# Performance work log

Measured on AMD Instinct MI355X. Metric: run time of the kernel, lower is better.

Reference implementation:

```python
import jax, jax.numpy as jnp
import numpy as np

TOP_K = 2
CAPACITY_FACTOR = 1.25
LOAD_BALANCE_WEIGHT = 0.01
ROUTER_Z_WEIGHT = 0.001


def setup_inputs() -> dict:
    key = jax.random.key(0)
    k1, k2, k3, k4, k5 = jax.random.split(key, 5)
    B, S, D, F, E = 4, 2048, 1024, 4096, 8
    x = jax.random.normal(k1, (B, S, D), dtype=jnp.float32)
    gate_w = jax.random.normal(k2, (E, D), dtype=jnp.float32) * 0.02
    wi_gate = jax.random.normal(k3, (E, F, D), dtype=jnp.float32) * 0.02
    wi_up = jax.random.normal(k4, (E, F, D), dtype=jnp.float32) * 0.02
    wo = jax.random.normal(k5, (E, D, F), dtype=jnp.float32) * 0.02
    return {"x": x, "gate_w": gate_w, "wi_gate": wi_gate, "wi_up": wi_up, "wo": wo}


def _dispatch_combine_one_k(x_flat, eids, ew, wi_gate, wi_up, wo, capacity):
    """Capacity-limited dispatch (first-come positions), GeGLU expert, combine."""
    N, D = x_flat.shape
    E = wi_gate.shape[0]
    # position of each token within its expert's queue (count of earlier tokens
    # assigned to the same expert) -- matches the atomic counter semantics in order.
    oh = jax.nn.one_hot(eids, E, dtype=jnp.int32)            # [N, E]
    pos = jnp.cumsum(oh, axis=0) - oh                        # counts strictly before
    pos = jnp.take_along_axis(pos, eids[:, None], axis=1)[:, 0]  # [N]
    valid = pos < capacity
    pos_safe = jnp.where(valid, pos, capacity)               # overflow bucket
    # dispatched_x[e, c, :] = x of the token at slot (e, c); zeros where empty
    disp = jnp.zeros((E, capacity + 1, D), x_flat.dtype).at[eids, pos_safe].set(x_flat)
    disp = disp[:, :capacity]                                # drop overflow bucket
    # grouped GeGLU expert: batched GEMMs over experts
    gate_h = jax.nn.silu(jnp.einsum('ecd,efd->ecf', disp, wi_gate))
    up_h = jnp.einsum('ecd,efd->ecf', disp, wi_up)
    eout = jnp.einsum('ecf,edf->ecd', gate_h * up_h, wo)     # [E, cap, D]
    # combine: gather each token's expert output, weight, zero dropped tokens
    y = eout[eids, jnp.minimum(pos, capacity - 1)]           # [N, D]
    return y * (ew * valid.astype(x_flat.dtype))[:, None]


def reference(x, gate_w, wi_gate, wi_up, wo):
    B, S, D = x.shape
    E = gate_w.shape[0]
    N = B * S
    capacity = max(int(N / E * CAPACITY_FACTOR), 1)
    x_flat = x.reshape(N, D)
    router_logits = x_flat @ gate_w.T                        # [N, E]
    router_probs = jax.nn.softmax(router_logits, axis=-1)
    topk_probs, topk_idx = jax.lax.top_k(router_probs, TOP_K)
    topk_probs = topk_probs / jnp.sum(topk_probs, axis=-1, keepdims=True)
    out = jnp.zeros_like(x_flat)
    for k in range(TOP_K):
        out = out + _dispatch_combine_one_k(
            x_flat, topk_idx[:, k], topk_probs[:, k], wi_gate, wi_up, wo, capacity)
    # aux losses: Switch-style load balance + router z-loss
    density = jnp.mean(jax.nn.one_hot(topk_idx, E, dtype=x.dtype).sum(axis=1), axis=0) / TOP_K
    mean_probs = jnp.mean(router_probs, axis=0)
    lb_loss = LOAD_BALANCE_WEIGHT * E * jnp.sum(density * mean_probs)
    z_loss = ROUTER_Z_WEIGHT * jnp.mean(jax.scipy.special.logsumexp(router_logits, axis=-1) ** 2)
    aux_loss = lb_loss + z_loss
    return out.reshape(B, S, D), aux_loss
```

## Files before the change

kernel.cpp:

```cpp
#include <hip/hip_runtime.h>
#include <cstdint>
#include <cstddef>

#define N_TOK 8192
#define DDIM  1024
#define FDIM  4096
#define NEXP  8
#define CAP   1280
#define MPE   2560
#define NSLOT (NEXP * MPE)

typedef __attribute__((ext_vector_type(8))) __bf16 bf16x8;
typedef __attribute__((ext_vector_type(4))) float  f32x4;

__device__ __forceinline__ unsigned short f2bf(float f) {
    unsigned int u = __float_as_uint(f);
    u += 0x7fffu + ((u >> 16) & 1u);
    return (unsigned short)(u >> 16);
}
__device__ __forceinline__ float bf2f(unsigned short s) {
    unsigned int u = ((unsigned int)s) << 16;
    return __uint_as_float(u);
}

__device__ __forceinline__ void async_cp16(const void* g, void* l) {
    __builtin_amdgcn_global_load_lds(
        (const __attribute__((address_space(1))) unsigned int*)g,
        (__attribute__((address_space(3))) unsigned int*)l, 16, 0, 0);
}

__global__ __launch_bounds__(256) void convert_wi_kernel(
    const float* __restrict__ wi_gate, const float* __restrict__ wi_up,
    unsigned short* __restrict__ wcomb)
{
    const int idx = blockIdx.x * 256 + threadIdx.x;
    const int d8 = idx & 127;
    const int r  = (idx >> 7) & 8191;
    const int e  = idx >> 20;
    const int f  = (r >> 7) * 64 + (r & 63);
    const float* src = (((r >> 6) & 1) ? wi_up : wi_gate)
                       + ((size_t)(e * FDIM + f) * DDIM + d8 * 8);
    const float4 a = ((const float4*)src)[0];
    const float4 b = ((const float4*)src)[1];
    uint4 o;
    o.x = (unsigned)f2bf(a.x) | ((unsigned)f2bf(a.y) << 16);
    o.y = (unsigned)f2bf(a.z) | ((unsigned)f2bf(a.w) << 16);
    o.z = (unsigned)f2bf(b.x) | ((unsigned)f2bf(b.y) << 16);
    o.w = (unsigned)f2bf(b.z) | ((unsigned)f2bf(b.w) << 16);
    *(uint4*)(wcomb + (size_t)idx * 8) = o;
}

__global__ __launch_bounds__(256) void convert_wo_kernel(
    const float* __restrict__ wo, unsigned short* __restrict__ wo_bf)
{
    const int idx = blockIdx.x * 256 + threadIdx.x;
    const float4 a = ((const float4*)(wo + (size_t)idx * 8))[0];
    const float4 b = ((const float4*)(wo + (size_t)idx * 8))[1];
    uint4 o;
    o.x = (unsigned)f2bf(a.x) | ((unsigned)f2bf(a.y) << 16);
    o.y = (unsigned)f2bf(a.z) | ((unsigned)f2bf(a.w) << 16);
    o.z = (unsigned)f2bf(b.x) | ((unsigned)f2bf(b.y) << 16);
    o.w = (unsigned)f2bf(b.z) | ((unsigned)f2bf(b.w) << 16);
    *(uint4*)(wo_bf + (size_t)idx * 8) = o;
}

__global__ __launch_bounds__(256) void router_kernel(
    const float* __restrict__ x, const float* __restrict__ gate_w,
    int* __restrict__ topk_idx, float* __restrict__ topk_w,
    float* __restrict__ stats)
{
    __shared__ float red[256][9];
    const int n = blockIdx.x;
    const int t = threadIdx.x;
    const float4 xv = *(const float4*)(x + (size_t)n * DDIM + t * 4);
#pragma unroll
    for (int e = 0; e < NEXP; e++) {
        const float4 gv = *(const float4*)(gate_w + (size_t)e * DDIM + t * 4);
        red[t][e] = xv.x * gv.x + xv.y * gv.y + xv.z * gv.z + xv.w * gv.w;
    }
    __syncthreads();
    for (int s = 128; s > 0; s >>= 1) {
        if (t < s) {
#pragma unroll
            for (int e = 0; e < NEXP; e++) red[t][e] += red[t + s][e];
        }
        __syncthreads();
    }
    if (t == 0) {
        float l[NEXP], p[NEXP];
        float m = -1e30f;
#pragma unroll
        for (int e = 0; e < NEXP; e++) { l[e] = red[0][e]; m = fmaxf(m, l[e]); }
        float sum = 0.f;
#pragma unroll
        for (int e = 0; e < NEXP; e++) { p[e] = expf(l[e] - m); sum += p[e]; }
        const float inv = 1.f / sum;
#pragma unroll
        for (int e = 0; e < NEXP; e++) p[e] *= inv;
        const float lse = m + logf(sum);
        int e1 = 0; float p1 = p[0];
#pragma unroll
        for (int e = 1; e < NEXP; e++) if (p[e] > p1) { p1 = p[e]; e1 = e; }
        int e2 = -1; float p2 = -1.f;
#pragma unroll
        for (int e = 0; e < NEXP; e++) if (e != e1 && p[e] > p2) { p2 = p[e]; e2 = e; }
        const float wsum = p1 + p2;
        topk_idx[n * 2 + 0] = e1; topk_idx[n * 2 + 1] = e2;
        topk_w[n * 2 + 0] = p1 / wsum; topk_w[n * 2 + 1] = p2 / wsum;
        float* sp = stats + (n & 63) * 17;
#pragma unroll
        for (int e = 0; e < NEXP; e++) atomicAdd(sp + e, p[e]);
        atomicAdd(sp + 8 + e1, 1.f);
        atomicAdd(sp + 8 + e2, 1.f);
        atomicAdd(sp + 16, lse * lse);
    }
}

__global__ __launch_bounds__(512) void pos_kernel(
    const int* __restrict__ topk_idx, const float* __restrict__ topk_w,
    int* __restrict__ slot_tok, float* __restrict__ w_slot, int* __restrict__ gcnt)
{
    __shared__ int cnt[2][NEXP][256];
    const int t = threadIdx.x;
    for (int i = t; i < NSLOT; i += 512) { slot_tok[i] = -1; w_slot[i] = 0.f; }
    const int kk = t >> 8;
    const int c  = t & 255;
    int lc[NEXP];
#pragma unroll
    for (int e = 0; e < NEXP; e++) lc[e] = 0;
    const int base_n = c * 32;
    for (int i = 0; i < 32; i++) lc[topk_idx[(base_n + i) * 2 + kk]]++;
#pragma unroll
    for (int e = 0; e < NEXP; e++) cnt[kk][e][c] = lc[e];
    __syncthreads();
    if (t < 16) {
        const int k2 = t >> 3, e = t & 7;
        int run = 0;
        for (int c2 = 0; c2 < 256; c2++) { int v = cnt[k2][e][c2]; cnt[k2][e][c2] = run; run += v; }
        gcnt[e * 2 + k2] = run < CAP ? run : CAP;
    }
    __syncthreads();
    int run[NEXP];
#pragma unroll
    for (int e = 0; e < NEXP; e++) run[e] = cnt[kk][e][c];
    for (int i = 0; i < 32; i++) {
        const int n = base_n + i;
        const int e = topk_idx[n * 2 + kk];
        const int p = run[e]++;
        if (p < CAP) {
            const int slot = (e * 2 + kk) * CAP + p;
            slot_tok[slot] = n;
            w_slot[slot] = topk_w[n * 2 + kk];
        }
    }
}

__global__ __launch_bounds__(128) void dispatch_kernel(
    const float* __restrict__ x, const int* __restrict__ slot_tok,
    unsigned short* __restrict__ disp)
{
    const int slot = blockIdx.x;
    const int t = threadIdx.x;
    const int token = slot_tok[slot];
    uint4 o = make_uint4(0u, 0u, 0u, 0u);
    if (token >= 0) {
        const float4* src = (const float4*)(x + (size_t)token * DDIM + t * 8);
        const float4 a = src[0];
        const float4 b = src[1];
        o.x = (unsigned)f2bf(a.x) | ((unsigned)f2bf(a.y) << 16);
        o.y = (unsigned)f2bf(a.z) | ((unsigned)f2bf(a.w) << 16);
        o.z = (unsigned)f2bf(b.x) | ((unsigned)f2bf(b.y) << 16);
        o.w = (unsigned)f2bf(b.z) | ((unsigned)f2bf(b.w) << 16);
    }
    *(uint4*)(disp + (size_t)slot * DDIM + t * 8) = o;
}

__global__ __launch_bounds__(256, 3) void gemm1_kernel(
    const unsigned short* __restrict__ disp,
    const unsigned short* __restrict__ wcomb,
    const int* __restrict__ gcnt,
    unsigned short* __restrict__ act)
{
    __shared__ __align__(16) unsigned short smem[8192];
    const int b = blockIdx.x;
    const int e   = b / 1280;
    const int rem = b % 1280;
    const int mb = rem / 64, nb = rem % 64;
    const int kk = mb / 10;
    if ((mb % 10) * 128 >= gcnt[e * 2 + kk]) return;

    const int t = threadIdx.x;
    const int wave = t >> 6, lane = t & 63;
    const unsigned short* Asrc = disp  + (size_t)(e * MPE + mb * 128) * DDIM;
    const unsigned short* Bsrc = wcomb + (size_t)e * 8192 * DDIM + (size_t)(nb * 128) * DDIM;

    const int arow = t >> 2;
    const int acol = (t & 3) * 8;

    const f32x4 fzero = {0.f, 0.f, 0.f, 0.f};
    f32x4 acc[4][4];
#pragma unroll
    for (int i = 0; i < 4; i++)
#pragma unroll
        for (int j = 0; j < 4; j++) acc[i][j] = fzero;

    const int wm = wave >> 1, wn = wave & 1;
    const int lrow = lane & 15, lk = lane >> 4;

    for (int k0 = 0; k0 < DDIM; k0 += 32) {
        __syncthreads();
        async_cp16(Asrc + (size_t)arow * DDIM + k0 + acol,        &smem[wave * 512]);
        async_cp16(Asrc + (size_t)(arow + 64) * DDIM + k0 + acol, &smem[2048 + wave * 512]);
        async_cp16(Bsrc + (size_t)arow * DDIM + k0 + acol,        &smem[4096 + wave * 512]);
        async_cp16(Bsrc + (size_t)(arow + 64) * DDIM + k0 + acol, &smem[6144 + wave * 512]);
        __syncthreads();
        bf16x8 af[4], bfr[4];
#pragma unroll
        for (int i = 0; i < 4; i++)
            af[i] = *(const bf16x8*)&smem[(wm * 64 + i * 16 + lrow) * 32 + lk * 8];
#pragma unroll
        for (int j = 0; j < 4; j++)
            bfr[j] = *(const bf16x8*)&smem[4096 + (wn * 64 + j * 16 + lrow) * 32 + lk * 8];
#pragma unroll
        for (int i = 0; i < 4; i++)
#pragma unroll
            for (int j = 0; j < 4; j++)
                acc[i][j] = __builtin_amdgcn_mfma_f32_16x16x32_bf16(af[i], bfr[j], acc[i][j], 0, 0, 0);
    }

    __syncthreads();
    if (wn == 0) {
#pragma unroll
        for (int i = 0; i < 4; i++)
#pragma unroll
            for (int j = 0; j < 4; j++)
#pragma unroll
                for (int r = 0; r < 4; r++)
                    smem[(wm * 64 + i * 16 + lk * 4 + r) * 64 + j * 16 + lrow] = f2bf(acc[i][j][r]);
    }
    __syncthreads();
    if (wn == 1) {
#pragma unroll
        for (int i = 0; i < 4; i++)
#pragma unroll
            for (int r = 0; r < 4; r++) {
                const int m = wm * 64 + i * 16 + lk * 4 + r;
                const size_t base = (size_t)(e * MPE + mb * 128 + m) * FDIM + nb * 64;
#pragma unroll
                for (int j = 0; j < 4; j++) {
                    const float g = bf2f(smem[m * 64 + j * 16 + lrow]);
                    const float u = acc[i][j][r];
                    const float a = (g / (1.f + __expf(-g))) * u;
                    act[base + j * 16 + lrow] = f2bf(a);
                }
            }
    }
}

__global__ __launch_bounds__(256, 3) void gemm2_kernel(
    const unsigned short* __restrict__ act,
    const unsigned short* __restrict__ wo_bf,
    const int* __restrict__ slot_tok, const float* __restrict__ w_slot,
    const int* __restrict__ gcnt,
    float* __restrict__ out)
{
    __shared__ __align__(16) unsigned short smem[8192];
    const int b = blockIdx.x;
    const int e   = b / 160;
    const int rem = b % 160;
    const int mb = rem / 8, nb = rem % 8;
    const int kk = mb / 10;
    if ((mb % 10) * 128 >= gcnt[e * 2 + kk]) return;

    const int t = threadIdx.x;
    const int wave = t >> 6, lane = t & 63;
    const unsigned short* Asrc = act   + (size_t)(e * MPE + mb * 128) * FDIM;
    const unsigned short* Bsrc = wo_bf + (size_t)e * DDIM * FDIM + (size_t)(nb * 128) * FDIM;

    const int arow = t >> 2;
    const int acol = (t & 3) * 8;

    const f32x4 fzero = {0.f, 0.f, 0.f, 0.f};
    f32x4 acc[4][4];
#pragma unroll
    for (int i = 0; i < 4; i++)
#pragma unroll
        for (int j = 0; j < 4; j++) acc[i][j] = fzero;

    const int wm = wave >> 1, wn = wave & 1;
    const int lrow = lane & 15, lk = lane >> 4;

    for (int k0 = 0; k0 < FDIM; k0 += 32) {
        __syncthreads();
        async_cp16(Asrc + (size_t)arow * FDIM + k0 + acol,        &smem[wave * 512]);
        async_cp16(Asrc + (size_t)(arow + 64) * FDIM + k0 + acol, &smem[2048 + wave * 512]);
        async_cp16(Bsrc + (size_t)arow * FDIM + k0 + acol,        &smem[4096 + wave * 512]);
        async_cp16(Bsrc + (size_t)(arow + 64) * FDIM + k0 + acol, &smem[6144 + wave * 512]);
        __syncthreads();
        bf16x8 af[4], bfr[4];
#pragma unroll
        for (int i = 0; i < 4; i++)
            af[i] = *(const bf16x8*)&smem[(wm * 64 + i * 16 + lrow) * 32 + lk * 8];
#pragma unroll
        for (int j = 0; j < 4; j++)
            bfr[j] = *(const bf16x8*)&smem[4096 + (wn * 64 + j * 16 + lrow) * 32 + lk * 8];
#pragma unroll
        for (int i = 0; i < 4; i++)
#pragma unroll
            for (int j = 0; j < 4; j++)
                acc[i][j] = __builtin_amdgcn_mfma_f32_16x16x32_bf16(af[i], bfr[j], acc[i][j], 0, 0, 0);
    }
#pragma unroll
    for (int i = 0; i < 4; i++)
#pragma unroll
        for (int r = 0; r < 4; r++) {
            const int srow = e * MPE + mb * 128 + wm * 64 + i * 16 + lk * 4 + r;
            const int token = slot_tok[srow];
            if (token >= 0) {
                const float w = w_slot[srow];
                const size_t obase = (size_t)token * DDIM + nb * 128 + wn * 64 + lrow;
#pragma unroll
                for (int j = 0; j < 4; j++)
                    atomicAdd(&out[obase + j * 16], acc[i][j][r] * w);
            }
        }
}

__global__ void aux_kernel(const float* __restrict__ stats, float* __restrict__ out)
{
    if (threadIdx.x == 0 && blockIdx.x == 0) {
        float ps[NEXP], cn[NEXP], z = 0.f;
#pragma unroll
        for (int e = 0; e < NEXP; e++) { ps[e] = 0.f; cn[e] = 0.f; }
        for (int c = 0; c < 64; c++) {
            const float* sp = stats + c * 17;
#pragma unroll
            for (int e = 0; e < NEXP; e++) { ps[e] += sp[e]; cn[e] += sp[8 + e]; }
            z += sp[16];
        }
        float lb = 0.f;
#pragma unroll
        for (int e = 0; e < NEXP; e++)
            lb += (cn[e] / (2.f * N_TOK)) * (ps[e] / N_TOK);
        const float aux = 0.01f * 8.f * lb + 0.001f * (z / N_TOK);
        out[(size_t)N_TOK * DDIM] = aux;
    }
}

extern "C" void kernel_launch(void* const* d_in, const int* in_sizes, int n_in,
                              void* d_out, int out_size, void* d_ws, size_t ws_size,
                              hipStream_t stream)
{
    (void)in_sizes; (void)n_in; (void)ws_size;
    const float* x       = (const float*)d_in[0];
    const float* gate_w  = (const float*)d_in[1];
    const float* wi_gate = (const float*)d_in[2];
    const float* wi_up   = (const float*)d_in[3];
    const float* wo      = (const float*)d_in[4];
    float* out = (float*)d_out;
    char* ws = (char*)d_ws;

    int*            topk_idx = (int*)(ws + 0);
    float*          topk_w   = (float*)(ws + 65536);
    int*            slot_tok = (int*)(ws + 131072);
    float*          w_slot   = (float*)(ws + 212992);
    float*          stats    = (float*)(ws + 294912);
    int*            gcnt     = (int*)(ws + 299264);
    unsigned short* disp     = (unsigned short*)(ws + 524288);
    unsigned short* act      = (unsigned short*)(ws + 42467328);
    unsigned short* wcomb    = (unsigned short*)(ws + 210239488);
    unsigned short* wo_bf    = (unsigned short*)(ws + 344457216);

    hipMemsetAsync(d_out, 0, (size_t)out_size * sizeof(float), stream);
    hipMemsetAsync(stats, 0, 64 * 17 * sizeof(float), stream);

    convert_wi_kernel<<<32768, 256, 0, stream>>>(wi_gate, wi_up, wcomb);
    convert_wo_kernel<<<16384, 256, 0, stream>>>(wo, wo_bf);
    router_kernel<<<N_TOK, 256, 0, stream>>>(x, gate_w, topk_idx, topk_w, stats);
    pos_kernel<<<1, 512, 0, stream>>>(topk_idx, topk_w, slot_tok, w_slot, gcnt);
    dispatch_kernel<<<NSLOT, 128, 0, stream>>>(x, slot_tok, disp);
    gemm1_kernel<<<NEXP * 20 * 64, 256, 0, stream>>>(disp, wcomb, gcnt, act);
    gemm2_kernel<<<NEXP * 20 * 8, 256, 0, stream>>>(act, wo_bf, slot_tok, w_slot, gcnt, out);
    aux_kernel<<<1, 64, 0, stream>>>(stats, out);
}
```

Measured before the change: 1.146 ms.

## Replace atomic combine with bf16 expert output and gather combine kernel; swizzle LDS

gemm2 now writes expert outputs as bf16 to a slot-indexed buffer instead of doing fp32 atomicAdds into the output, and a new combine kernel gathers each token's two slots and applies the routing weights. This removes the output memset and the atomic contention. The router now uses one wave per token with shuffle reductions instead of a shared-memory tree. The GEMM kernels get an XOR swizzle on LDS columns and a padded epilogue stride to cut bank conflicts. The trade-off is an extra 40MB write and read of the expert outputs, plus bf16 rounding of those outputs.

New measurement: 1.112 ms. 1.03x faster.

```diff
diff --git a/kernel.cpp b/kernel.cpp
--- a/kernel.cpp
+++ b/kernel.cpp
@@ -19,8 +19,7 @@
     return (unsigned short)(u >> 16);
 }
 __device__ __forceinline__ float bf2f(unsigned short s) {
-    unsigned int u = ((unsigned int)s) << 16;
-    return __uint_as_float(u);
+    return __uint_as_float(((unsigned int)s) << 16);
 }
 
 __device__ __forceinline__ void async_cp16(const void* g, void* l) {
@@ -69,35 +68,40 @@
     int* __restrict__ topk_idx, float* __restrict__ topk_w,
     float* __restrict__ stats)
 {
-    __shared__ float red[256][9];
-    const int n = blockIdx.x;
-    const int t = threadIdx.x;
-    const float4 xv = *(const float4*)(x + (size_t)n * DDIM + t * 4);
+    const int wave = threadIdx.x >> 6, lane = threadIdx.x & 63;
+    const int n = blockIdx.x * 4 + wave;
+    const float4* xp = (const float4*)(x + (size_t)n * DDIM + lane * 16);
+    float4 xv[4];
+#pragma unroll
+    for (int i = 0; i < 4; i++) xv[i] = xp[i];
+    float part[NEXP];
 #pragma unroll
     for (int e = 0; e < NEXP; e++) {
-        const float4 gv = *(const float4*)(gate_w + (size_t)e * DDIM + t * 4);
-        red[t][e] = xv.x * gv.x + xv.y * gv.y + xv.z * gv.z + xv.w * gv.w;
-    }
-    __syncthreads();
-    for (int s = 128; s > 0; s >>= 1) {
-        if (t < s) {
-#pragma unroll
-            for (int e = 0; e < NEXP; e++) red[t][e] += red[t + s][e];
+        const float4* gp = (const float4*)(gate_w + (size_t)e * DDIM + lane * 16);
+        float s = 0.f;
+#pragma unroll
+        for (int i = 0; i < 4; i++) {
+            const float4 g = gp[i];
+            s += xv[i].x * g.x + xv[i].y * g.y + xv[i].z * g.z + xv[i].w * g.w;
         }
-        __syncthreads();
-    }
-    if (t == 0) {
-        float l[NEXP], p[NEXP];
+        part[e] = s;
+    }
+#pragma unroll
+    for (int off = 32; off > 0; off >>= 1)
+#pragma unroll
+        for (int e = 0; e < NEXP; e++) part[e] += __shfl_down(part[e], off);
+    if (lane == 0) {
+        float p[NEXP];
         float m = -1e30f;
 #pragma unroll
-        for (int e = 0; e < NEXP; e++) { l[e] = red[0][e]; m = fmaxf(m, l[e]); }
+        for (int e = 0; e < NEXP; e++) m = fmaxf(m, part[e]);
         float sum = 0.f;
 #pragma unroll
-        for (int e = 0; e < NEXP; e++) { p[e] = expf(l[e] - m); sum += p[e]; }
+        for (int e = 0; e < NEXP; e++) { p[e] = __expf(part[e] - m); sum += p[e]; }
         const float inv = 1.f / sum;
 #pragma unroll
         for (int e = 0; e < NEXP; e++) p[e] *= inv;
-        const float lse = m + logf(sum);
+        const float lse = m + __logf(sum);
         int e1 = 0; float p1 = p[0];
 #pragma unroll
         for (int e = 1; e < NEXP; e++) if (p[e] > p1) { p1 = p[e]; e1 = e; }
@@ -118,11 +122,11 @@
 
 __global__ __launch_bounds__(512) void pos_kernel(
     const int* __restrict__ topk_idx, const float* __restrict__ topk_w,
-    int* __restrict__ slot_tok, float* __restrict__ w_slot, int* __restrict__ gcnt)
+    int* __restrict__ slot_tok, int* __restrict__ tok2slot, int* __restrict__ gcnt)
 {
     __shared__ int cnt[2][NEXP][256];
     const int t = threadIdx.x;
-    for (int i = t; i < NSLOT; i += 512) { slot_tok[i] = -1; w_slot[i] = 0.f; }
+    for (int i = t; i < NSLOT; i += 512) slot_tok[i] = -1;
     const int kk = t >> 8;
     const int c  = t & 255;
     int lc[NEXP];
@@ -150,7 +154,9 @@
         if (p < CAP) {
             const int slot = (e * 2 + kk) * CAP + p;
             slot_tok[slot] = n;
-            w_slot[slot] = topk_w[n * 2 + kk];
+            tok2slot[n * 2 + kk] = slot;
+        } else {
+            tok2slot[n * 2 + kk] = -1;
         }
     }
 }
@@ -181,7 +187,7 @@
     const int* __restrict__ gcnt,
     unsigned short* __restrict__ act)
 {
-    __shared__ __align__(16) unsigned short smem[8192];
+    __shared__ __align__(16) unsigned short smem[8704];
     const int b = blockIdx.x;
     const int e   = b / 1280;
     const int rem = b % 1280;
@@ -195,7 +201,7 @@
     const unsigned short* Bsrc = wcomb + (size_t)e * 8192 * DDIM + (size_t)(nb * 128) * DDIM;
 
     const int arow = t >> 2;
-    const int acol = (t & 3) * 8;
+    const int acol = (((t & 3) ^ ((arow >> 1) & 3)) * 8);
 
     const f32x4 fzero = {0.f, 0.f, 0.f, 0.f};
     f32x4 acc[4][4];
@@ -206,6 +212,7 @@
 
     const int wm = wave >> 1, wn = wave & 1;
     const int lrow = lane & 15, lk = lane >> 4;
+    const int lkx = (lk ^ ((lrow >> 1) & 3)) * 8;
 
     for (int k0 = 0; k0 < DDIM; k0 += 32) {
         __syncthreads();
@@ -217,10 +224,10 @@
         bf16x8 af[4], bfr[4];
 #pragma unroll
         for (int i = 0; i < 4; i++)
-            af[i] = *(const bf16x8*)&smem[(wm * 64 + i * 16 + lrow) * 32 + lk * 8];
+            af[i] = *(const bf16x8*)&smem[(wm * 64 + i * 16 + lrow) * 32 + lkx];
 #pragma unroll
         for (int j = 0; j < 4; j++)
-            bfr[j] = *(const bf16x8*)&smem[4096 + (wn * 64 + j * 16 + lrow) * 32 + lk * 8];
+            bfr[j] = *(const bf16x8*)&smem[4096 + (wn * 64 + j * 16 + lrow) * 32 + lkx];
 #pragma unroll
         for (int i = 0; i < 4; i++)
 #pragma unroll
@@ -236,7 +243,7 @@
             for (int j = 0; j < 4; j++)
 #pragma unroll
                 for (int r = 0; r < 4; r++)
-                    smem[(wm * 64 + i * 16 + lk * 4 + r) * 64 + j * 16 + lrow] = f2bf(acc[i][j][r]);
+                    smem[(wm * 64 + i * 16 + lk * 4 + r) * 68 + j * 16 + lrow] = f2bf(acc[i][j][r]);
     }
     __syncthreads();
     if (wn == 1) {
@@ -248,7 +255,7 @@
                 const size_t base = (size_t)(e * MPE + mb * 128 + m) * FDIM + nb * 64;
 #pragma unroll
                 for (int j = 0; j < 4; j++) {
-                    const float g = bf2f(smem[m * 64 + j * 16 + lrow]);
+                    const float g = bf2f(smem[m * 68 + j * 16 + lrow]);
                     const float u = acc[i][j][r];
                     const float a = (g / (1.f + __expf(-g))) * u;
                     act[base + j * 16 + lrow] = f2bf(a);
@@ -260,9 +267,8 @@
 __global__ __launch_bounds__(256, 3) void gemm2_kernel(
     const unsigned short* __restrict__ act,
     const unsigned short* __restrict__ wo_bf,
-    const int* __restrict__ slot_tok, const float* __restrict__ w_slot,
     const int* __restrict__ gcnt,
-    float* __restrict__ out)
+    unsigned short* __restrict__ eout)
 {
     __shared__ __align__(16) unsigned short smem[8192];
     const int b = blockIdx.x;
@@ -278,7 +284,7 @@
     const unsigned short* Bsrc = wo_bf + (size_t)e * DDIM * FDIM + (size_t)(nb * 128) * FDIM;
 
     const int arow = t >> 2;
-    const int acol = (t & 3) * 8;
+    const int acol = (((t & 3) ^ ((arow >> 1) & 3)) * 8);
 
     const f32x4 fzero = {0.f, 0.f, 0.f, 0.f};
     f32x4 acc[4][4];
@@ -289,6 +295,7 @@
 
     const int wm = wave >> 1, wn = wave & 1;
     const int lrow = lane & 15, lk = lane >> 4;
+    const int lkx = (lk ^ ((lrow >> 1) & 3)) * 8;
 
     for (int k0 = 0; k0 < FDIM; k0 += 32) {
         __syncthreads();
@@ -300,10 +307,10 @@
         bf16x8 af[4], bfr[4];
 #pragma unroll
         for (int i = 0; i < 4; i++)
-            af[i] = *(const bf16x8*)&smem[(wm * 64 + i * 16 + lrow) * 32 + lk * 8];
+            af[i] = *(const bf16x8*)&smem[(wm * 64 + i * 16 + lrow) * 32 + lkx];
 #pragma unroll
         for (int j = 0; j < 4; j++)
-            bfr[j] = *(const bf16x8*)&smem[4096 + (wn * 64 + j * 16 + lrow) * 32 + lk * 8];
+            bfr[j] = *(const bf16x8*)&smem[4096 + (wn * 64 + j * 16 + lrow) * 32 + lkx];
 #pragma unroll
         for (int i = 0; i < 4; i++)
 #pragma unroll
@@ -315,15 +322,33 @@
 #pragma unroll
         for (int r = 0; r < 4; r++) {
             const int srow = e * MPE + mb * 128 + wm * 64 + i * 16 + lk * 4 + r;
-            const int token = slot_tok[srow];
-            if (token >= 0) {
-                const float w = w_slot[srow];
-                const size_t obase = (size_t)token * DDIM + nb * 128 + wn * 64 + lrow;
-#pragma unroll
-                for (int j = 0; j < 4; j++)
-                    atomicAdd(&out[obase + j * 16], acc[i][j][r] * w);
-            }
+            const size_t obase = (size_t)srow * DDIM + nb * 128 + wn * 64;
+#pragma unroll
+            for (int j = 0; j < 4; j++)
+                eout[obase + j * 16 + lrow] = f2bf(acc[i][j][r]);
         }
+}
+
+__global__ __launch_bounds__(256) void combine_kernel(
+    const unsigned short* __restrict__ eout,
+    const int* __restrict__ tok2slot, const float* __restrict__ topk_w,
+    float* __restrict__ out)
+{
+    const int n = blockIdx.x;
+    const int t = threadIdx.x;
+    const int s0 = tok2slot[n * 2 + 0], s1 = tok2slot[n * 2 + 1];
+    const float w0 = (s0 >= 0) ? topk_w[n * 2 + 0] : 0.f;
+    const float w1 = (s1 >= 0) ? topk_w[n * 2 + 1] : 0.f;
+    const int a0 = (s0 >= 0) ? s0 : 0;
+    const int a1 = (s1 >= 0) ? s1 : 0;
+    const uint2 p0 = *(const uint2*)(eout + (size_t)a0 * DDIM + t * 4);
+    const uint2 p1 = *(const uint2*)(eout + (size_t)a1 * DDIM + t * 4);
+    float4 o;
+    o.x = w0 * bf2f((unsigned short)(p0.x & 0xffff)) + w1 * bf2f((unsigned short)(p1.x & 0xffff));
+    o.y = w0 * bf2f((unsigned short)(p0.x >> 16))    + w1 * bf2f((unsigned short)(p1.x >> 16));
+    o.z = w0 * bf2f((unsigned short)(p0.y & 0xffff)) + w1 * bf2f((unsigned short)(p1.y & 0xffff));
+    o.w = w0 * bf2f((unsigned short)(p0.y >> 16))    + w1 * bf2f((unsigned short)(p1.y >> 16));
+    *(float4*)(out + (size_t)n * DDIM + t * 4) = o;
 }
 
 __global__ void aux_kernel(const float* __restrict__ stats, float* __restrict__ out)
@@ -351,7 +376,7 @@
                               void* d_out, int out_size, void* d_ws, size_t ws_size,
                               hipStream_t stream)
 {
-    (void)in_sizes; (void)n_in; (void)ws_size;
+    (void)in_sizes; (void)n_in; (void)ws_size; (void)out_size;
     const float* x       = (const float*)d_in[0];
     const float* gate_w  = (const float*)d_in[1];
     const float* wi_gate = (const float*)d_in[2];
@@ -363,23 +388,24 @@
     int*            topk_idx = (int*)(ws + 0);
     float*          topk_w   = (float*)(ws + 65536);
     int*            slot_tok = (int*)(ws + 131072);
-    float*          w_slot   = (float*)(ws + 212992);
-    float*          stats    = (float*)(ws + 294912);
-    int*            gcnt     = (int*)(ws + 299264);
+    int*            tok2slot = (int*)(ws + 212992);
+    float*          stats    = (float*)(ws + 278528);
+    int*            gcnt     = (int*)(ws + 282880);
     unsigned short* disp     = (unsigned short*)(ws + 524288);
     unsigned short* act      = (unsigned short*)(ws + 42467328);
-    unsigned short* wcomb    = (unsigned short*)(ws + 210239488);
-    unsigned short* wo_bf    = (unsigned short*)(ws + 344457216);
-
-    hipMemsetAsync(d_out, 0, (size_t)out_size * sizeof(float), stream);
+    unsigned short* eout     = (unsigned short*)(ws + 210239488);
+    unsigned short* wcomb    = (unsigned short*)(ws + 252182528);
+    unsigned short* wo_bf    = (unsigned short*)(ws + 386400256);
+
     hipMemsetAsync(stats, 0, 64 * 17 * sizeof(float), stream);
 
     convert_wi_kernel<<<32768, 256, 0, stream>>>(wi_gate, wi_up, wcomb);
     convert_wo_kernel<<<16384, 256, 0, stream>>>(wo, wo_bf);
-    router_kernel<<<N_TOK, 256, 0, stream>>>(x, gate_w, topk_idx, topk_w, stats);
-    pos_kernel<<<1, 512, 0, stream>>>(topk_idx, topk_w, slot_tok, w_slot, gcnt);
+    router_kernel<<<N_TOK / 4, 256, 0, stream>>>(x, gate_w, topk_idx, topk_w, stats);
+    pos_kernel<<<1, 512, 0, stream>>>(topk_idx, topk_w, slot_tok, tok2slot, gcnt);
     dispatch_kernel<<<NSLOT, 128, 0, stream>>>(x, slot_tok, disp);
     gemm1_kernel<<<NEXP * 20 * 64, 256, 0, stream>>>(disp, wcomb, gcnt, act);
-    gemm2_kernel<<<NEXP * 20 * 8, 256, 0, stream>>>(act, wo_bf, slot_tok, w_slot, gcnt, out);
+    gemm2_kernel<<<NEXP * 20 * 8, 256, 0, stream>>>(act, wo_bf, gcnt, eout);
+    combine_kernel<<<N_TOK, 256, 0, stream>>>(eout, tok2slot, topk_w, out);
     aux_kernel<<<1, 64, 0, stream>>>(stats, out);
 }
```
